# Kernel tuning notes

Measured on AMD Instinct MI355X. Metric: run time of the kernel, lower is better.

## Reference

```python
import jax, jax.numpy as jnp
import numpy as np

E, H, G = 1024, 16, 1          # embed_dim, num_heads, gqa_factor
HKV = H // G                   # kv heads
D = E // H                     # head_dim
EKV = HKV * D                  # kv_embed_dim
B, TQ, TK = 4, 512, 1024
CLAMP = float(-np.log(1.0 / 0.98 - 1.0))  # neg_prob_to_phi(clamp_prob=0.98)
SCALE = float(1.0 / np.sqrt(D))           # 1/norm_fact
NEG = -1e30                                # ~ -inf in log space


def monotonic_attention(phi):
    """Log-space monotonic alignment DP over the last axis.
    phi: (N, Ti, Tj) clamped transition logits. Returns log alignment probs, same shape.
    alpha[i,0] = 0 if i==0 else -inf
    alpha[i,j] = logaddexp(alpha[i,j-1] + logsigmoid(phi[i,j-1]),      # stay at row i
                           alpha[i-1,j-1] + logsigmoid(-phi[i-1,j-1])) # advance to row i
    """
    log_p = jax.nn.log_sigmoid(phi)
    log_1mp = jax.nn.log_sigmoid(-phi)
    N, Ti, Tj = phi.shape
    alpha0 = jnp.full((N, Ti), NEG, phi.dtype).at[:, 0].set(0.0)
    neg_col = jnp.full((N, 1), NEG, phi.dtype)

    def step(alpha, cols):
        lp, l1mp = cols  # each (N, Ti)
        stay = alpha + lp
        move = jnp.concatenate([neg_col, (alpha + l1mp)[:, :-1]], axis=1)
        new = jnp.logaddexp(stay, move)
        return new, new

    xs = (jnp.moveaxis(log_p[:, :, :-1], -1, 0), jnp.moveaxis(log_1mp[:, :, :-1], -1, 0))
    _, rest = jax.lax.scan(step, alpha0, xs)             # (Tj-1, N, Ti)
    alphas = jnp.concatenate([alpha0[None], rest], axis=0)  # (Tj, N, Ti)
    return jnp.moveaxis(alphas, 0, -1)                   # (N, Ti, Tj)


def setup_inputs() -> dict:
    k = jax.random.key(0)
    ks = jax.random.split(k, 5)
    bw = float(np.sqrt(6.0 / ((2 * E + 2 * EKV) + E)))  # xavier_uniform bound
    bo = float(1.0 / np.sqrt(E))                        # nn.Linear default bound
    return {
        "query": jax.random.normal(ks[0], (B, TQ, E), jnp.float32),
        "key": jax.random.normal(ks[1], (B, TK, E), jnp.float32),
        "value": jax.random.normal(ks[2], (B, TK, E), jnp.float32),
        "in_proj_weight": jax.random.uniform(ks[3], (2 * E + 2 * EKV, E), jnp.float32, -bw, bw),
        "in_proj_bias": jnp.zeros((2 * E + 2 * EKV,), jnp.float32),
        "out_w": jax.random.uniform(ks[4], (E, E), jnp.float32, -bo, bo),
        "out_b": jnp.zeros((E,), jnp.float32),
    }


def reference(query, key, value, in_proj_weight, in_proj_bias, out_w, out_b):
    qwa, qw, kw, vw = jnp.split(in_proj_weight, [E, 2 * E, 2 * E + EKV], axis=0)
    qba, qb, kb, vb = jnp.split(in_proj_bias, [E, 2 * E, 2 * E + EKV])

    def proj(x, w, b, g):
        y = x @ w.T + b
        Bx, T, _ = x.shape
        return y.reshape(Bx, T, g, HKV, D).transpose(0, 2, 3, 1, 4)  # (B,g,HKV,T,D)

    xqa = proj(query, qwa, qba, G)  # monotonic query
    xq = proj(query, qw, qb, G)     # regular query
    xk = proj(key, kw, kb, 1)
    xv = proj(value, vw, vb, 1)

    # mode = 'many_keys_one_query': DP grid has key rows, query cols
    phi = jnp.einsum('bghqc,bghkc->bghkq', xqa, xk)
    phi = jnp.tanh(phi) * CLAMP  # soft clamp
    mono = monotonic_attention(phi.reshape(-1, TK, TQ)).reshape(B, G, HKV, TK, TQ)
    mono = jnp.swapaxes(mono, -2, -1)  # (B,G,H,TQ,TK)

    reg = jnp.einsum('bghqc,bghkc->bghqk', xq, xk) * SCALE
    attn = jax.nn.softmax(reg + mono, axis=-1)
    xo = jnp.einsum('bghqk,bghkc->bghqc', attn, xv)
    xo = xo.transpose(0, 3, 1, 2, 4).reshape(B, TQ, E)
    return xo @ out_w.T + out_b
```

## Files before the change

kernel.cpp:

```cpp
#include <hip/hip_runtime.h>
#include <hip/hip_fp16.h>
#include <hip/hip_bf16.h>
#include <math.h>

typedef unsigned short u16;
typedef __attribute__((ext_vector_type(8))) short bf16x8;
typedef __attribute__((ext_vector_type(8))) unsigned short u16x8;
typedef __attribute__((ext_vector_type(4))) unsigned short u16x4;
typedef __attribute__((ext_vector_type(4))) float f32x4;

static constexpr float CLAMPF = 3.8918202981106265f;
static constexpr float SCALEF = 0.125f;
static constexpr float ASCALE = 16384.f;

__device__ __forceinline__ u16 f2bf(float x) {
    __hip_bfloat16 h = __float2bfloat16(x);
    return *reinterpret_cast<u16*>(&h);
}

__global__ __launch_bounds__(256)
void cvt_all_k(const float* __restrict__ q, const float* __restrict__ key,
               const float* __restrict__ val, const float* __restrict__ W,
               const float* __restrict__ ow,
               u16* __restrict__ QBF, u16* __restrict__ KBF,
               u16* __restrict__ VBF, u16* __restrict__ WBF,
               u16* __restrict__ OWBF)
{
    long i = (long)blockIdx.x * 256 + threadIdx.x;
    float4 v;
    u16* dst; long off;
    if (i < 524288) {
        dst = QBF; off = i;
        v = ((const float4*)q)[i];
    } else if (i < 1048576) {
        off = i - 524288;
        long r = off >> 8, c4 = off & 255;
        long b = r >> 9, tok = r & 511;
        dst = KBF;
        v = ((const float4*)key)[(b * 1024 + tok) * 256 + c4];
    } else if (i < 1572864) {
        off = i - 1048576;
        long r = off >> 8, c4 = off & 255;
        long b = r >> 9, tok = r & 511;
        dst = VBF;
        v = ((const float4*)val)[(b * 1024 + tok) * 256 + c4];
    } else if (i < 2621440) {
        dst = WBF; off = i - 1572864;
        v = ((const float4*)W)[off];
    } else if (i < 2883584) {
        dst = OWBF; off = i - 2621440;
        v = ((const float4*)ow)[off];
    } else return;
    u16x4 o; o.x = f2bf(v.x); o.y = f2bf(v.y); o.z = f2bf(v.z); o.w = f2bf(v.w);
    ((u16x4*)dst)[off] = o;
}

template<int TM, int TN, int EPI, bool TRI>
__device__ __forceinline__
void mfma_body(u16* As, u16* Bs, int bx, int by, int bz,
               const u16* __restrict__ Ag, const u16* __restrict__ Bg,
               void* __restrict__ Cg, const float* __restrict__ bias,
               int K, int lda, int ldb, int ldc,
               long sAb, long sAh, long sBb, long sBh, long sCb, long sCh,
               int hdiv)
{
    int b = bz / hdiv, h = bz % hdiv;
    const u16* A = Ag + (long)b * sAb + (long)h * sAh;
    const u16* B = Bg + (long)b * sBb + (long)h * sBh;

    int tid = threadIdx.x;
    int bm = by * TM, bn = bx * TN;

    constexpr int AC = TM / 32;
    constexpr int BC = TN / 32;
    int srow = tid >> 3;
    int scol = (tid & 7) * 8;

    int wid = tid >> 6, lane = tid & 63;
    int wr = wid >> 1, wc = wid & 1;
    constexpr int MI = TM / 32;
    constexpr int NI = TN / 32;
    int arow0 = wr * (TM / 2) + (lane & 15);
    int bcol0 = wc * (TN / 2) + (lane & 15);
    int koff = (lane >> 4) * 8;

    if constexpr (TRI) {
        if (bx > by) {
            __half* C = (__half*)Cg + (long)b * sCb + (long)h * sCh;
            int rb = bm + wr * (TM / 2) + (lane >> 4) * 4;
            int cb = bn + wc * (TN / 2) + (lane & 15);
            __half z16 = __float2half(0.f);
#pragma unroll
            for (int mi = 0; mi < MI; ++mi)
#pragma unroll
                for (int ni = 0; ni < NI; ++ni)
#pragma unroll
                    for (int r = 0; r < 4; ++r)
                        C[(long)(rb + 16 * mi + r) * ldc + cb + 16 * ni] = z16;
            return;
        }
    }

    f32x4 acc[MI][NI];
#pragma unroll
    for (int i = 0; i < MI; ++i)
#pragma unroll
        for (int j = 0; j < NI; ++j) acc[i][j] = (f32x4){0.f, 0.f, 0.f, 0.f};

    for (int kt = 0; kt < K; kt += 64) {
        u16x8 av[AC], bv[BC];
#pragma unroll
        for (int c = 0; c < AC; ++c)
            av[c] = *(const u16x8*)(A + (long)(bm + srow + 32 * c) * lda + kt + scol);
#pragma unroll
        for (int c = 0; c < BC; ++c)
            bv[c] = *(const u16x8*)(B + (long)(bn + srow + 32 * c) * ldb + kt + scol);
        __syncthreads();
#pragma unroll
        for (int c = 0; c < AC; ++c)
            *(u16x8*)&As[(srow + 32 * c) * 64 + scol] = av[c];
#pragma unroll
        for (int c = 0; c < BC; ++c)
            *(u16x8*)&Bs[(srow + 32 * c) * 64 + scol] = bv[c];
        __syncthreads();

#pragma unroll
        for (int ks = 0; ks < 2; ++ks) {
            bf16x8 af[MI], bfr[NI];
#pragma unroll
            for (int mi = 0; mi < MI; ++mi)
                af[mi] = *(const bf16x8*)&As[(arow0 + 16 * mi) * 64 + ks * 32 + koff];
#pragma unroll
            for (int ni = 0; ni < NI; ++ni)
                bfr[ni] = *(const bf16x8*)&Bs[(bcol0 + 16 * ni) * 64 + ks * 32 + koff];
#pragma unroll
            for (int mi = 0; mi < MI; ++mi)
#pragma unroll
                for (int ni = 0; ni < NI; ++ni)
                    acc[mi][ni] = __builtin_amdgcn_mfma_f32_16x16x32_bf16(
                        af[mi], bfr[ni], acc[mi][ni], 0, 0, 0);
        }
    }

    int rbase = bm + wr * (TM / 2) + (lane >> 4) * 4;
    int cbase = bn + wc * (TN / 2) + (lane & 15);
#pragma unroll
    for (int mi = 0; mi < MI; ++mi) {
#pragma unroll
        for (int ni = 0; ni < NI; ++ni) {
            int m0 = rbase + 16 * mi;
            int n = cbase + 16 * ni;
            if constexpr (EPI == 0) {
                u16* C = (u16*)Cg + (long)b * sCb + (long)h * sCh;
                float bvv = bias ? bias[n] : 0.f;
#pragma unroll
                for (int r = 0; r < 4; ++r)
                    C[(long)(m0 + r) * ldc + n] = f2bf(acc[mi][ni][r] + bvv);
            } else if constexpr (EPI == 1) {
                __half* C = (__half*)Cg + (long)b * sCb + (long)h * sCh;
#pragma unroll
                for (int r = 0; r < 4; ++r) {
                    float x = acc[mi][ni][r];
                    float e2 = __expf(2.f * x);
                    float tv = CLAMPF - (2.f * CLAMPF) * __builtin_amdgcn_rcpf(e2 + 1.f);
                    float pv = __builtin_amdgcn_rcpf(1.f + __expf(-tv));
                    C[(long)(m0 + r) * ldc + n] = __float2half(pv);
                }
            } else if constexpr (EPI == 3) {
                float* C = (float*)Cg + (long)b * sCb + (long)h * sCh;
                float bvv = bias[n];
#pragma unroll
                for (int r = 0; r < 4; ++r)
                    C[(long)(m0 + r) * ldc + n] = acc[mi][ni][r] + bvv;
            } else {
                u16* C = (u16*)Cg;
                float bvv = bias[n];
                long vaddr = ((long)(b * 16 + (n >> 6)) * 64 + (n & 63)) * 512 + m0;
                u16x4 pk;
                pk.x = f2bf(acc[mi][ni][0] + bvv);
                pk.y = f2bf(acc[mi][ni][1] + bvv);
                pk.z = f2bf(acc[mi][ni][2] + bvv);
                pk.w = f2bf(acc[mi][ni][3] + bvv);
                *(u16x4*)(C + vaddr) = pk;
            }
        }
    }
}

template<int TM, int TN, int EPI, bool TRI = false>
__global__ __launch_bounds__(256)
void mfma_nt(const u16* __restrict__ Ag, const u16* __restrict__ Bg,
             void* __restrict__ Cg, const float* __restrict__ bias,
             int K, int lda, int ldb, int ldc,
             long sAb, long sAh, long sBb, long sBh, long sCb, long sCh,
             int hdiv)
{
    __shared__ u16 As[TM * 64];
    __shared__ u16 Bs[TN * 64];
    mfma_body<TM, TN, EPI, TRI>(As, Bs, blockIdx.x, blockIdx.y, blockIdx.z,
                                Ag, Bg, Cg, bias, K, lda, ldb, ldc,
                                sAb, sAh, sBb, sBh, sCb, sCh, hdiv);
}

__global__ __launch_bounds__(256)
void proj_qk_k(const u16* __restrict__ QBF, const u16* __restrict__ KBF,
               const u16* __restrict__ WBF, const float* __restrict__ ipb,
               u16* __restrict__ XQAQ, u16* __restrict__ XK)
{
    __shared__ u16 As[128 * 64];
    __shared__ u16 Bs[128 * 64];
    int bid = blockIdx.x;
    if (bid < 128) {
        mfma_body<128, 128, 0, false>(As, Bs, bid & 7, bid >> 3, 0,
            QBF, WBF, XQAQ, ipb, 1024, 1024, 1024, 2048, 0, 0, 0, 0, 0, 0, 1);
    } else {
        int idx = bid - 128;
        mfma_body<128, 128, 0, false>(As, Bs, idx & 7, (idx >> 3) & 3, idx >> 5,
            KBF, WBF + 2097152, XK, ipb + 2048, 1024, 1024, 1024, 1024,
            524288L, 0, 0, 0, 524288L, 0, 1);
    }
}

#define DPL8(J) (*(const uint4*)(p + (long)min((J), 510) * 512 + k0))

#define DSTEP(PC, J) do { \
    const __half2* hp = (const __half2*)&(PC); \
    float pv[8]; \
    { float2 q01 = __half22float2(hp[0]); pv[0] = q01.x; pv[1] = q01.y; } \
    { float2 q23 = __half22float2(hp[1]); pv[2] = q23.x; pv[3] = q23.y; } \
    { float2 q45 = __half22float2(hp[2]); pv[4] = q45.x; pv[5] = q45.y; } \
    { float2 q67 = __half22float2(hp[3]); pv[6] = q67.x; pv[7] = q67.y; } \
    float c[8]; \
    _Pragma("unroll") \
    for (int r = 0; r < 8; ++r) c[r] = fmaf(-a[r], pv[r], a[r]); \
    float cp = __shfl_up(c[7], 1, 64); \
    if (lane == 0) cp = 0.f; \
    a[0] = fmaf(a[0], pv[0], cp); \
    _Pragma("unroll") \
    for (int r = 1; r < 8; ++r) a[r] = fmaf(a[r], pv[r], c[r - 1]); \
    uint4 st; \
    { __half2 h0 = __floats2half2_rn(a[0], a[1]), h1 = __floats2half2_rn(a[2], a[3]); \
      st.x = *(unsigned*)&h0; st.y = *(unsigned*)&h1; } \
    { __half2 h2 = __floats2half2_rn(a[4], a[5]), h3 = __floats2half2_rn(a[6], a[7]); \
      st.z = *(unsigned*)&h2; st.w = *(unsigned*)&h3; } \
    *(uint4*)(al + (long)(J) * 512 + k0) = st; \
} while (0)

__global__ __launch_bounds__(256)
void dp_v_k(const __half* __restrict__ P, __half* __restrict__ AL,
            const u16* __restrict__ QBF, const u16* __restrict__ VBF,
            const u16* __restrict__ WBF, const float* __restrict__ ipb,
            u16* __restrict__ XQAQ, u16* __restrict__ VT)
{
    __shared__ u16 As[128 * 64];
    __shared__ u16 Bs[128 * 64];
    int bid = blockIdx.x;

    if (bid >= 192) {
        int idx = bid - 192;
        mfma_body<128, 128, 0, false>(As, Bs, 8 + (idx & 7), idx >> 3, 0,
            QBF, WBF, XQAQ, ipb, 1024, 1024, 1024, 2048, 0, 0, 0, 0, 0, 0, 1);
        return;
    }
    if (bid >= 64) {
        int idx = bid - 64;
        mfma_body<128, 128, 4, false>(As, Bs, idx & 7, (idx >> 3) & 3, idx >> 5,
            VBF, WBF + 3145728, VT, ipb + 3072, 1024, 1024, 1024, 0,
            524288L, 0, 0, 0, 0, 0, 1);
        return;
    }

    if (threadIdx.x >= 64) return;
    int n = bid;
    int lane = threadIdx.x;
    const __half* p = P + (long)n * 262144;
    __half* al = AL + (long)n * 262144;
    int k0 = lane * 8;

    float a[8];
#pragma unroll
    for (int r = 0; r < 8; ++r) a[r] = 0.f;
    if (lane == 0) a[0] = ASCALE;
    {
        uint4 st;
        __half2 h0 = __floats2half2_rn(a[0], a[1]), h1 = __floats2half2_rn(a[2], a[3]);
        __half2 h2 = __floats2half2_rn(a[4], a[5]), h3 = __floats2half2_rn(a[6], a[7]);
        st.x = *(unsigned*)&h0; st.y = *(unsigned*)&h1;
        st.z = *(unsigned*)&h2; st.w = *(unsigned*)&h3;
        *(uint4*)(al + k0) = st;
    }

    int j = 1;
    uint4 f0 = DPL8(0), f1 = DPL8(1), f2 = DPL8(2), f3 = DPL8(3);
    uint4 f4 = DPL8(4), f5 = DPL8(5), f6 = DPL8(6), f7 = DPL8(7);

    while (j + 7 < 512) {
        DSTEP(f0, j); f0 = DPL8(j + 7); ++j;
        DSTEP(f1, j); f1 = DPL8(j + 7); ++j;
        DSTEP(f2, j); f2 = DPL8(j + 7); ++j;
        DSTEP(f3, j); f3 = DPL8(j + 7); ++j;
        DSTEP(f4, j); f4 = DPL8(j + 7); ++j;
        DSTEP(f5, j); f5 = DPL8(j + 7); ++j;
        DSTEP(f6, j); f6 = DPL8(j + 7); ++j;
        DSTEP(f7, j); f7 = DPL8(j + 7); ++j;
    }
    while (j < 512) {
        DSTEP(f0, j);
        f0 = f1; f1 = f2; f2 = f3; f3 = f4; f4 = f5; f5 = f6; f6 = f7;
        ++j;
    }
}

__global__ __launch_bounds__(256, 4)
void fused_attn_k(const u16* __restrict__ XQAQ, const u16* __restrict__ XK,
                  const u16* __restrict__ VT, const __half* __restrict__ AL,
                  u16* __restrict__ XO)
{
    __shared__ u16 wtile[4][2048];
    __shared__ float co[4][16][64];
    __shared__ float cml[4][2][16];

    int n = blockIdx.x; int b = n >> 4, h = n & 15;
    int tid = threadIdx.x, wave = tid >> 6, lane = tid & 63;
    int l15 = lane & 15, l4 = lane >> 4;
    int qg = blockIdx.y * 16;
    u16* wlds = wtile[wave];
    int swz = (l15 & 7) << 3;

    float m = -3.0e38f, lsum = 0.f;
    f32x4 o[4];
#pragma unroll
    for (int df = 0; df < 4; ++df) o[df] = (f32x4){0.f, 0.f, 0.f, 0.f};

    if (wave * 128 < qg + 16) {
        const u16* qbase = XQAQ + (long)(b * 512 + qg + l15) * 2048 + 1024 + h * 64 + l4 * 8;
        bf16x8 qf0 = *(const bf16x8*)(qbase);
        bf16x8 qf1 = *(const bf16x8*)(qbase + 32);

        const u16* kbase = XK + (long)(b * 512 + wave * 128 + l15) * 1024 + h * 64 + l4 * 8;
        const __half* abase = AL + (long)(n * 512 + qg + l15) * 512 + wave * 128 + l4 * 4;
        const u16* vbase = VT + (long)(n * 64 + l15) * 512 + wave * 128 + l4 * 8;

        uint2 areg[8];
#pragma unroll
        for (int kf = 0; kf < 8; ++kf)
            areg[kf] = *(const uint2*)(abase + kf * 16);

        f32x4 s[8];
#pragma unroll
        for (int kf = 0; kf < 8; ++kf) {
            const u16* kb = kbase + (long)(kf * 16) * 1024;
            bf16x8 k0 = *(const bf16x8*)kb;
            bf16x8 k1 = *(const bf16x8*)(kb + 32);
            f32x4 acc = (f32x4){0.f, 0.f, 0.f, 0.f};
            acc = __builtin_amdgcn_mfma_f32_16x16x32_bf16(k0, qf0, acc, 0, 0, 0);
            acc = __builtin_amdgcn_mfma_f32_16x16x32_bf16(k1, qf1, acc, 0, 0, 0);
            s[kf] = acc;
        }

        float mt = -3.0e38f;
#pragma unroll
        for (int kf = 0; kf < 8; ++kf)
            mt = fmaxf(mt, fmaxf(fmaxf(s[kf][0], s[kf][1]), fmaxf(s[kf][2], s[kf][3])));
        mt = fmaxf(mt, __shfl_xor(mt, 16, 64));
        mt = fmaxf(mt, __shfl_xor(mt, 32, 64));
        m = mt;
        float negm = -mt * SCALEF;

#pragma unroll
        for (int kf = 0; kf < 8; ++kf) {
            float2 a01 = __half22float2(*(__half2*)&areg[kf].x);
            float2 a23 = __half22float2(*(__half2*)&areg[kf].y);
            float w0 = a01.x * __expf(fmaf(s[kf][0], SCALEF, negm));
            float w1 = a01.y * __expf(fmaf(s[kf][1], SCALEF, negm));
            float w2 = a23.x * __expf(fmaf(s[kf][2], SCALEF, negm));
            float w3 = a23.y * __expf(fmaf(s[kf][3], SCALEF, negm));
            lsum += (w0 + w1) + (w2 + w3);
            u16x4 wp; wp.x = f2bf(w0); wp.y = f2bf(w1); wp.z = f2bf(w2); wp.w = f2bf(w3);
            *(u16x4*)&wlds[(l15 * 128 + kf * 16 + l4 * 4) ^ swz] = wp;
        }

#pragma unroll
        for (int ks2 = 0; ks2 < 4; ++ks2) {
            bf16x8 wf = *(const bf16x8*)&wlds[(l15 * 128 + ks2 * 32 + l4 * 8) ^ swz];
#pragma unroll
            for (int df = 0; df < 4; ++df) {
                const u16* vb = vbase + (long)(df * 16) * 512 + ks2 * 32;
                bf16x8 vf = *(const bf16x8*)vb;
                o[df] = __builtin_amdgcn_mfma_f32_16x16x32_bf16(wf, vf, o[df], 0, 0, 0);
            }
        }

        lsum += __shfl_xor(lsum, 16, 64);
        lsum += __shfl_xor(lsum, 32, 64);
    }

    if (lane < 16) { cml[wave][0][l15] = m; cml[wave][1][l15] = lsum; }
#pragma unroll
    for (int df = 0; df < 4; ++df)
#pragma unroll
        for (int r = 0; r < 4; ++r)
            co[wave][l4 * 4 + r][df * 16 + l15] = o[df][r];
    __syncthreads();

    int q = tid >> 4, d0 = (tid & 15) * 4;
    float m0 = cml[0][0][q], m1 = cml[1][0][q], m2 = cml[2][0][q], m3 = cml[3][0][q];
    float ms = fmaxf(fmaxf(m0, m1), fmaxf(m2, m3));
    float c0w = __expf((m0 - ms) * SCALEF), c1w = __expf((m1 - ms) * SCALEF);
    float c2w = __expf((m2 - ms) * SCALEF), c3w = __expf((m3 - ms) * SCALEF);
    float lt = c0w * cml[0][1][q] + c1w * cml[1][1][q]
             + c2w * cml[2][1][q] + c3w * cml[3][1][q];
    f32x4 o0 = *(const f32x4*)&co[0][q][d0];
    f32x4 o1 = *(const f32x4*)&co[1][q][d0];
    f32x4 o2 = *(const f32x4*)&co[2][q][d0];
    f32x4 o3 = *(const f32x4*)&co[3][q][d0];
    float inv = __builtin_amdgcn_rcpf(lt);
    u16x4 st;
#pragma unroll
    for (int j = 0; j < 4; ++j)
        st[j] = f2bf((c0w * o0[j] + c1w * o1[j] + c2w * o2[j] + c3w * o3[j]) * inv);
    *(u16x4*)&XO[(long)(b * 512 + qg + q) * 1024 + h * 64 + d0] = st;
}

extern "C" void kernel_launch(void* const* d_in, const int* in_sizes, int n_in,
                              void* d_out, int out_size, void* d_ws, size_t ws_size,
                              hipStream_t stream)
{
    const float* q   = (const float*)d_in[0];
    const float* key = (const float*)d_in[1];
    const float* val = (const float*)d_in[2];
    const float* W   = (const float*)d_in[3];
    const float* ipb = (const float*)d_in[4];
    const float* ow  = (const float*)d_in[5];
    const float* ob  = (const float*)d_in[6];
    float* out = (float*)d_out;
    char* w = (char*)d_ws;

    __half* PSIG  = (__half*)(w);
    __half* ALPHA = (__half*)(w + 33554432);
    u16*    XQAQ  = (u16*)(w + 67108864);
    u16*    XK    = (u16*)(w + 75497472);
    u16*    VT    = (u16*)(w + 79691776);
    u16*    XO    = (u16*)(w + 83886080);
    u16*    OWBF  = (u16*)(w + 88080384);
    u16*    KBF   = (u16*)(w + 90177536);
    u16*    VBF   = (u16*)(w + 94371840);
    u16*    WBF   = (u16*)(w + 98566144);
    u16*    QBF   = (u16*)(w + 83886080);

    dim3 blk(256);

    cvt_all_k<<<dim3(11264), blk, 0, stream>>>(
        q, key, val, W, ow, QBF, KBF, VBF, WBF, OWBF);

    proj_qk_k<<<dim3(256), blk, 0, stream>>>(QBF, KBF, WBF, ipb, XQAQ, XK);

    mfma_nt<128, 128, 1, true><<<dim3(4, 4, 64), blk, 0, stream>>>(
        XQAQ, XK, PSIG, nullptr, 64, 2048, 1024, 512,
        1048576L, 64, 524288L, 64, 4194304L, 262144L, 16);

    dp_v_k<<<dim3(320), blk, 0, stream>>>(PSIG, ALPHA, QBF, VBF, WBF, ipb, XQAQ, VT);

    fused_attn_k<<<dim3(64, 32, 1), blk, 0, stream>>>(XQAQ, XK, VT, ALPHA, XO);

    mfma_nt<128, 128, 3><<<dim3(8, 16, 1), blk, 0, stream>>>(
        XO, OWBF, out, ob, 1024, 1024, 1024, 1024, 0, 0, 0, 0, 0, 0, 1);
}
```

Measured before the change: 160.9 us.

## Parallelize monotonic DP scan via chunked banded transfer operators

```diff
diff --git a/kernel.cpp b/kernel.cpp
--- a/kernel.cpp
+++ b/kernel.cpp
@@ -221,15 +221,181 @@
     }
 }
 
-#define DPL8(J) (*(const uint4*)(p + (long)min((J), 510) * 512 + k0))
-
-#define DSTEP(PC, J) do { \
+
+__global__ __launch_bounds__(64)
+void dpA_k(const __half* __restrict__ P, __half* __restrict__ BND)
+{
+    int g = blockIdx.x;
+    int n = blockIdx.y;
+    int lane = threadIdx.x;
+    const __half* p = P + (long)n * 262144;
+    int k0 = lane * 8;
+
+    float band[8][9];
+#pragma unroll
+    for (int r = 0; r < 8; ++r)
+#pragma unroll
+        for (int d = 0; d < 9; ++d) band[r][d] = 0.f;
+
+    {
+        uint4 pc4 = *(const uint4*)(p + (long)(8 * g) * 512 + k0);
+        const __half2* hp = (const __half2*)&pc4;
+        float pc[8];
+        { float2 t = __half22float2(hp[0]); pc[0] = t.x; pc[1] = t.y; }
+        { float2 t = __half22float2(hp[1]); pc[2] = t.x; pc[3] = t.y; }
+        { float2 t = __half22float2(hp[2]); pc[4] = t.x; pc[5] = t.y; }
+        { float2 t = __half22float2(hp[3]); pc[6] = t.x; pc[7] = t.y; }
+        float p7s = __shfl_up(pc[7], 1, 64);
+#pragma unroll
+        for (int r = 0; r < 8; ++r) band[r][0] = pc[r];
+        band[0][1] = (lane == 0) ? 0.f : (1.f - p7s);
+#pragma unroll
+        for (int r = 1; r < 8; ++r) band[r][1] = 1.f - pc[r - 1];
+    }
+
+    for (int s = 1; s < 8; ++s) {
+        uint4 pc4 = *(const uint4*)(p + (long)(8 * g + s) * 512 + k0);
+        const __half2* hp = (const __half2*)&pc4;
+        float pc[8];
+        { float2 t = __half22float2(hp[0]); pc[0] = t.x; pc[1] = t.y; }
+        { float2 t = __half22float2(hp[1]); pc[2] = t.x; pc[3] = t.y; }
+        { float2 t = __half22float2(hp[2]); pc[4] = t.x; pc[5] = t.y; }
+        { float2 t = __half22float2(hp[3]); pc[6] = t.x; pc[7] = t.y; }
+        float p7s = __shfl_up(pc[7], 1, 64);
+        float qm0 = (lane == 0) ? 0.f : (1.f - p7s);
+        float qm[8];
+        qm[0] = qm0;
+#pragma unroll
+        for (int r = 1; r < 8; ++r) qm[r] = 1.f - pc[r - 1];
+        float prev7[9];
+#pragma unroll
+        for (int d = 0; d < 9; ++d) {
+            float v = __shfl_up(band[7][d], 1, 64);
+            prev7[d] = (lane == 0) ? 0.f : v;
+        }
+#pragma unroll
+        for (int r = 7; r >= 1; --r) {
+#pragma unroll
+            for (int d = 8; d >= 1; --d)
+                band[r][d] = fmaf(qm[r], band[r - 1][d - 1], pc[r] * band[r][d]);
+            band[r][0] = pc[r] * band[r][0];
+        }
+#pragma unroll
+        for (int d = 8; d >= 1; --d)
+            band[0][d] = fmaf(qm0, prev7[d - 1], pc[0] * band[0][d]);
+        band[0][0] = pc[0] * band[0][0];
+    }
+
+    long gb = (long)(n * 63 + g) * 9 * 512;
+#pragma unroll
+    for (int d = 0; d < 9; ++d) {
+        uint4 st;
+        __half2 h0 = __floats2half2_rn(band[0][d], band[1][d]);
+        __half2 h1 = __floats2half2_rn(band[2][d], band[3][d]);
+        __half2 h2 = __floats2half2_rn(band[4][d], band[5][d]);
+        __half2 h3 = __floats2half2_rn(band[6][d], band[7][d]);
+        st.x = *(unsigned*)&h0; st.y = *(unsigned*)&h1;
+        st.z = *(unsigned*)&h2; st.w = *(unsigned*)&h3;
+        *(uint4*)(BND + gb + (long)d * 512 + k0) = st;
+    }
+}
+
+__global__ __launch_bounds__(256)
+void dpB_misc_k(const __half* __restrict__ BND, float* __restrict__ BSTATE,
+                const u16* __restrict__ QBF, const u16* __restrict__ VBF,
+                const u16* __restrict__ WBF, const float* __restrict__ ipb,
+                u16* __restrict__ XQAQ, u16* __restrict__ VT)
+{
+    __shared__ u16 As[128 * 64];
+    __shared__ u16 Bs[128 * 64];
+    int bid = blockIdx.x;
+
+    if (bid >= 192) {
+        int idx = bid - 192;
+        mfma_body<128, 128, 0, false>(As, Bs, 8 + (idx & 7), idx >> 3, 0,
+            QBF, WBF, XQAQ, ipb, 1024, 1024, 1024, 2048, 0, 0, 0, 0, 0, 0, 1);
+        return;
+    }
+    if (bid >= 64) {
+        int idx = bid - 64;
+        mfma_body<128, 128, 4, false>(As, Bs, idx & 7, (idx >> 3) & 3, idx >> 5,
+            VBF, WBF + 3145728, VT, ipb + 3072, 1024, 1024, 1024, 0,
+            524288L, 0, 0, 0, 0, 0, 1);
+        return;
+    }
+
+    if (threadIdx.x >= 64) return;
+    int n = bid;
+    int lane = threadIdx.x;
+    int k0 = lane * 8;
+    const __half* bnd = BND + (long)n * 63 * 9 * 512;
+    float* bst = BSTATE + (long)n * 64 * 512;
+
+    float b[8];
+#pragma unroll
+    for (int r = 0; r < 8; ++r) b[r] = 0.f;
+    if (lane == 0) b[0] = ASCALE;
+    {
+        float4 v0; v0.x = b[0]; v0.y = b[1]; v0.z = b[2]; v0.w = b[3];
+        float4 v1; v1.x = b[4]; v1.y = b[5]; v1.z = b[6]; v1.w = b[7];
+        *(float4*)(bst + k0) = v0;
+        *(float4*)(bst + k0 + 4) = v1;
+    }
+
+    uint4 cur[9], nxt[9];
+#pragma unroll
+    for (int d = 0; d < 9; ++d)
+        cur[d] = *(const uint4*)(bnd + (long)d * 512 + k0);
+
+    for (int g = 0; g < 63; ++g) {
+        if (g + 1 < 63) {
+#pragma unroll
+            for (int d = 0; d < 9; ++d)
+                nxt[d] = *(const uint4*)(bnd + ((long)(g + 1) * 9 + d) * 512 + k0);
+        }
+        float pb[8];
+#pragma unroll
+        for (int r = 0; r < 8; ++r) {
+            float v = __shfl_up(b[r], 1, 64);
+            pb[r] = (lane == 0) ? 0.f : v;
+        }
+        float bn[8];
+#pragma unroll
+        for (int r = 0; r < 8; ++r) bn[r] = 0.f;
+#pragma unroll
+        for (int d = 0; d < 9; ++d) {
+            const __half2* hp = (const __half2*)&cur[d];
+            float f[8];
+            { float2 t = __half22float2(hp[0]); f[0] = t.x; f[1] = t.y; }
+            { float2 t = __half22float2(hp[1]); f[2] = t.x; f[3] = t.y; }
+            { float2 t = __half22float2(hp[2]); f[4] = t.x; f[5] = t.y; }
+            { float2 t = __half22float2(hp[3]); f[6] = t.x; f[7] = t.y; }
+#pragma unroll
+            for (int r = 0; r < 8; ++r) {
+                float src = (r - d >= 0) ? b[r - d] : pb[8 + r - d];
+                bn[r] = fmaf(f[r], src, bn[r]);
+            }
+        }
+#pragma unroll
+        for (int r = 0; r < 8; ++r) b[r] = bn[r];
+        {
+            float4 v0; v0.x = b[0]; v0.y = b[1]; v0.z = b[2]; v0.w = b[3];
+            float4 v1; v1.x = b[4]; v1.y = b[5]; v1.z = b[6]; v1.w = b[7];
+            *(float4*)(bst + (long)(g + 1) * 512 + k0) = v0;
+            *(float4*)(bst + (long)(g + 1) * 512 + k0 + 4) = v1;
+        }
+#pragma unroll
+        for (int d = 0; d < 9; ++d) cur[d] = nxt[d];
+    }
+}
+
+#define CSTEP(PC, J) do { \
     const __half2* hp = (const __half2*)&(PC); \
     float pv[8]; \
-    { float2 q01 = __half22float2(hp[0]); pv[0] = q01.x; pv[1] = q01.y; } \
-    { float2 q23 = __half22float2(hp[1]); pv[2] = q23.x; pv[3] = q23.y; } \
-    { float2 q45 = __half22float2(hp[2]); pv[4] = q45.x; pv[5] = q45.y; } \
-    { float2 q67 = __half22float2(hp[3]); pv[6] = q67.x; pv[7] = q67.y; } \
+    { float2 t = __half22float2(hp[0]); pv[0] = t.x; pv[1] = t.y; } \
+    { float2 t = __half22float2(hp[1]); pv[2] = t.x; pv[3] = t.y; } \
+    { float2 t = __half22float2(hp[2]); pv[4] = t.x; pv[5] = t.y; } \
+    { float2 t = __half22float2(hp[3]); pv[6] = t.x; pv[7] = t.y; } \
     float c[8]; \
     _Pragma("unroll") \
     for (int r = 0; r < 8; ++r) c[r] = fmaf(-a[r], pv[r], a[r]); \
@@ -246,42 +412,26 @@
     *(uint4*)(al + (long)(J) * 512 + k0) = st; \
 } while (0)
 
-__global__ __launch_bounds__(256)
-void dp_v_k(const __half* __restrict__ P, __half* __restrict__ AL,
-            const u16* __restrict__ QBF, const u16* __restrict__ VBF,
-            const u16* __restrict__ WBF, const float* __restrict__ ipb,
-            u16* __restrict__ XQAQ, u16* __restrict__ VT)
-{
-    __shared__ u16 As[128 * 64];
-    __shared__ u16 Bs[128 * 64];
-    int bid = blockIdx.x;
-
-    if (bid >= 192) {
-        int idx = bid - 192;
-        mfma_body<128, 128, 0, false>(As, Bs, 8 + (idx & 7), idx >> 3, 0,
-            QBF, WBF, XQAQ, ipb, 1024, 1024, 1024, 2048, 0, 0, 0, 0, 0, 0, 1);
-        return;
-    }
-    if (bid >= 64) {
-        int idx = bid - 64;
-        mfma_body<128, 128, 4, false>(As, Bs, idx & 7, (idx >> 3) & 3, idx >> 5,
-            VBF, WBF + 3145728, VT, ipb + 3072, 1024, 1024, 1024, 0,
-            524288L, 0, 0, 0, 0, 0, 1);
-        return;
-    }
-
-    if (threadIdx.x >= 64) return;
-    int n = bid;
+__global__ __launch_bounds__(64)
+void dpC_k(const __half* __restrict__ P, const float* __restrict__ BSTATE,
+           __half* __restrict__ AL)
+{
+    int g = blockIdx.x;
+    int n = blockIdx.y;
     int lane = threadIdx.x;
     const __half* p = P + (long)n * 262144;
     __half* al = AL + (long)n * 262144;
     int k0 = lane * 8;
+    const float* bst = BSTATE + ((long)n * 64 + g) * 512;
 
     float a[8];
-#pragma unroll
-    for (int r = 0; r < 8; ++r) a[r] = 0.f;
-    if (lane == 0) a[0] = ASCALE;
     {
+        float4 v0 = *(const float4*)(bst + k0);
+        float4 v1 = *(const float4*)(bst + k0 + 4);
+        a[0] = v0.x; a[1] = v0.y; a[2] = v0.z; a[3] = v0.w;
+        a[4] = v1.x; a[5] = v1.y; a[6] = v1.z; a[7] = v1.w;
+    }
+    if (g == 0) {
         uint4 st;
         __half2 h0 = __floats2half2_rn(a[0], a[1]), h1 = __floats2half2_rn(a[2], a[3]);
         __half2 h2 = __floats2half2_rn(a[4], a[5]), h3 = __floats2half2_rn(a[6], a[7]);
@@ -290,25 +440,26 @@
         *(uint4*)(al + k0) = st;
     }
 
-    int j = 1;
-    uint4 f0 = DPL8(0), f1 = DPL8(1), f2 = DPL8(2), f3 = DPL8(3);
-    uint4 f4 = DPL8(4), f5 = DPL8(5), f6 = DPL8(6), f7 = DPL8(7);
-
-    while (j + 7 < 512) {
-        DSTEP(f0, j); f0 = DPL8(j + 7); ++j;
-        DSTEP(f1, j); f1 = DPL8(j + 7); ++j;
-        DSTEP(f2, j); f2 = DPL8(j + 7); ++j;
-        DSTEP(f3, j); f3 = DPL8(j + 7); ++j;
-        DSTEP(f4, j); f4 = DPL8(j + 7); ++j;
-        DSTEP(f5, j); f5 = DPL8(j + 7); ++j;
-        DSTEP(f6, j); f6 = DPL8(j + 7); ++j;
-        DSTEP(f7, j); f7 = DPL8(j + 7); ++j;
-    }
-    while (j < 512) {
-        DSTEP(f0, j);
-        f0 = f1; f1 = f2; f2 = f3; f3 = f4; f4 = f5; f5 = f6; f6 = f7;
-        ++j;
-    }
+    int t0 = 8 * g + 1;
+    int nt = 511 - 8 * g; if (nt > 8) nt = 8;
+
+    uint4 f0 = *(const uint4*)(p + (long)min(8 * g + 0, 510) * 512 + k0);
+    uint4 f1 = *(const uint4*)(p + (long)min(8 * g + 1, 510) * 512 + k0);
+    uint4 f2 = *(const uint4*)(p + (long)min(8 * g + 2, 510) * 512 + k0);
+    uint4 f3 = *(const uint4*)(p + (long)min(8 * g + 3, 510) * 512 + k0);
+    uint4 f4 = *(const uint4*)(p + (long)min(8 * g + 4, 510) * 512 + k0);
+    uint4 f5 = *(const uint4*)(p + (long)min(8 * g + 5, 510) * 512 + k0);
+    uint4 f6 = *(const uint4*)(p + (long)min(8 * g + 6, 510) * 512 + k0);
+    uint4 f7 = *(const uint4*)(p + (long)min(8 * g + 7, 510) * 512 + k0);
+
+    CSTEP(f0, t0 + 0);
+    CSTEP(f1, t0 + 1);
+    CSTEP(f2, t0 + 2);
+    CSTEP(f3, t0 + 3);
+    CSTEP(f4, t0 + 4);
+    CSTEP(f5, t0 + 5);
+    CSTEP(f6, t0 + 6);
+    if (nt == 8) CSTEP(f7, t0 + 7);
 }
 
 __global__ __launch_bounds__(256, 4)
@@ -436,17 +587,19 @@
     float* out = (float*)d_out;
     char* w = (char*)d_ws;
 
-    __half* PSIG  = (__half*)(w);
-    __half* ALPHA = (__half*)(w + 33554432);
-    u16*    XQAQ  = (u16*)(w + 67108864);
-    u16*    XK    = (u16*)(w + 75497472);
-    u16*    VT    = (u16*)(w + 79691776);
-    u16*    XO    = (u16*)(w + 83886080);
-    u16*    OWBF  = (u16*)(w + 88080384);
-    u16*    KBF   = (u16*)(w + 90177536);
-    u16*    VBF   = (u16*)(w + 94371840);
-    u16*    WBF   = (u16*)(w + 98566144);
-    u16*    QBF   = (u16*)(w + 83886080);
+    __half* PSIG   = (__half*)(w);
+    u16*    XQAQ   = (u16*)(w + 33554432);
+    u16*    XK     = (u16*)(w + 41943040);
+    u16*    VT     = (u16*)(w + 46137344);
+    u16*    XO     = (u16*)(w + 50331648);
+    u16*    OWBF   = (u16*)(w + 54525952);
+    u16*    KBF    = (u16*)(w + 56623104);
+    u16*    VBF    = (u16*)(w + 60817408);
+    u16*    WBF    = (u16*)(w + 65011712);
+    float*  BSTATE = (float*)(w + 73400320);
+    __half* ALPHA  = (__half*)(w + 81788928);
+    __half* BND    = (__half*)(w + 81788928);
+    u16*    QBF    = (u16*)(w + 50331648);
 
     dim3 blk(256);
 
@@ -459,7 +612,12 @@
         XQAQ, XK, PSIG, nullptr, 64, 2048, 1024, 512,
         1048576L, 64, 524288L, 64, 4194304L, 262144L, 16);
 
-    dp_v_k<<<dim3(320), blk, 0, stream>>>(PSIG, ALPHA, QBF, VBF, WBF, ipb, XQAQ, VT);
+    dpA_k<<<dim3(63, 64), dim3(64), 0, stream>>>(PSIG, BND);
+
+    dpB_misc_k<<<dim3(320), blk, 0, stream>>>(
+        BND, BSTATE, QBF, VBF, WBF, ipb, XQAQ, VT);
+
+    dpC_k<<<dim3(64, 64), dim3(64), 0, stream>>>(PSIG, BSTATE, ALPHA);
 
     fused_attn_k<<<dim3(64, 32, 1), blk, 0, stream>>>(XQAQ, XK, VT, ALPHA, XO);
 
```

Measured after the change: 175.2 us. 1.09x slower.
